# Performance work log

Measured on AMD Instinct MI355X. Metric: run time of the kernel, lower is better.

## Reference

```python
import jax, jax.numpy as jnp
import numpy as np

T, B, IN_DIM, H = 512, 256, 512, 256  # H == hidden_dim == n_qubits

def setup_inputs() -> dict:
    key = jax.random.key(0)
    ks = jax.random.split(key, 13)
    inputs = jax.random.normal(ks[0], (T, B, IN_DIM), dtype=jnp.float32)
    d = IN_DIM + H
    s = 1.0 / np.sqrt(d)
    def lin(k):
        k1, k2 = jax.random.split(k)
        return (jax.random.uniform(k1, (H, d), jnp.float32, -s, s),
                jax.random.uniform(k2, (H,), jnp.float32, -s, s))
    Wf, bf = lin(ks[1]); Wi, bi = lin(ks[2]); Wg, bg = lin(ks[3]); Wo, bo = lin(ks[4])
    thf = jax.random.uniform(ks[5], (H,), jnp.float32)
    thi = jax.random.uniform(ks[6], (H,), jnp.float32)
    thg = jax.random.uniform(ks[7], (H,), jnp.float32)
    tho = jax.random.uniform(ks[8], (H,), jnp.float32)
    return dict(inputs=inputs, Wf=Wf, bf=bf, thf=thf, Wi=Wi, bi=bi, thi=thi,
                Wg=Wg, bg=bg, thg=thg, Wo=Wo, bo=bo, tho=tho)

def _qgate(combined, W, b, th):
    # Analytic form of the RY+RY+CNOT-ladder circuit with PauliZ expvals:
    # <Z_k> = prod_{i<=k} cos(z_i + theta_i), z = Linear(combined)
    z = combined @ W.T + b  # [B, H]
    return jnp.cumprod(jnp.cos(z + th), axis=-1)

def reference(inputs, Wf, bf, thf, Wi, bi, thi, Wg, bg, thg, Wo, bo, tho):
    batch = inputs.shape[1]
    hx0 = jnp.zeros((batch, H), inputs.dtype)
    cx0 = jnp.zeros((batch, H), inputs.dtype)

    def step(carry, x):
        hx, cx = carry
        comb = jnp.concatenate([x, hx], axis=1)  # [B, IN_DIM+H]
        f = jax.nn.sigmoid(_qgate(comb, Wf, bf, thf))
        i = jax.nn.sigmoid(_qgate(comb, Wi, bi, thi))
        g = jnp.tanh(_qgate(comb, Wg, bg, thg))
        o = jax.nn.sigmoid(_qgate(comb, Wo, bo, tho))
        cx = f * cx + i * g
        hx = o * jnp.tanh(cx)
        return (hx, cx), hx

    (hx, cx), stacked = jax.lax.scan(step, (hx0, cx0), inputs)
    return stacked, hx, cx
```

## Files before the change

### kernel.cpp

```cpp
#include <hip/hip_runtime.h>
#include <hip/hip_bf16.h>
#include <stdint.h>

#define T_STEPS 512
#define BATCH   256
#define HID     256

#define NRWG   128
#define NWWG   128
#define NWG    256
#define RING   4
#define CHUNK  8
#define NCHUNK 64
#define TPC    64
#define SLOT_F (CHUNK*256*1024)

using short8 = __attribute__((ext_vector_type(8))) short;
using f32x4  = __attribute__((ext_vector_type(4))) float;

#define VMCNT0() asm volatile("s_waitcnt vmcnt(0)" ::: "memory")

__device__ inline unsigned short f2bf(float f) {
  unsigned u = __float_as_uint(f);
  unsigned r = (u + 0x7fffu + ((u >> 16) & 1u)) >> 16;
  return (unsigned short)r;
}
__device__ inline float sigm(float x)   { return __builtin_amdgcn_rcpf(1.0f + __expf(-x)); }
__device__ inline float tanh_f(float x) { return 2.0f * __builtin_amdgcn_rcpf(1.0f + __expf(-2.0f * x)) - 1.0f; }

__device__ inline int ld_rlx(const int* p) {
  return __hip_atomic_load(p, __ATOMIC_RELAXED, __HIP_MEMORY_SCOPE_AGENT);
}
__device__ inline void add_rlx(int* p, int v) {
  __hip_atomic_fetch_add(p, v, __ATOMIC_RELAXED, __HIP_MEMORY_SCOPE_AGENT);
}
__device__ inline float ldg_coh(const float* p) {
  return __hip_atomic_load(p, __ATOMIC_RELAXED, __HIP_MEMORY_SCOPE_AGENT);
}
__device__ inline void stg_coh(float* p, float v) {
  __hip_atomic_store(p, v, __ATOMIC_RELAXED, __HIP_MEMORY_SCOPE_AGENT);
}
__device__ inline void st16_coh(float* p, f32x4 v) {
  asm volatile("global_store_dwordx4 %0, %1, off sc0 sc1" :: "v"(p), "v"(v) : "memory");
}

__device__ inline int hswz(int byte) { return byte ^ (((byte >> 8) & 3) << 4); }

__global__ __launch_bounds__(256) void prep_kernel(
    const float* __restrict__ Wf, const float* __restrict__ Wi,
    const float* __restrict__ Wg, const float* __restrict__ Wo,
    const float* __restrict__ bf_, const float* __restrict__ bi_,
    const float* __restrict__ bg_, const float* __restrict__ bo_,
    const float* __restrict__ thf, const float* __restrict__ thi,
    const float* __restrict__ thg, const float* __restrict__ tho,
    unsigned short* __restrict__ Wfull, float* __restrict__ cvec,
    int* __restrict__ flags, float* __restrict__ pk)
{
  int j = blockIdx.x;
  int g = j >> 8, col = j & 255;
  const float* W  = (g==0)?Wf:(g==1)?Wi:(g==2)?Wg:Wo;
  const float* bb = (g==0)?bf_:(g==1)?bi_:(g==2)?bg_:bo_;
  const float* th = (g==0)?thf:(g==1)?thi:(g==2)?thg:tho;
  const float* wrow = W + (size_t)col * 768;
  for (int k = threadIdx.x; k < 768; k += blockDim.x)
    Wfull[(size_t)j * 768 + k] = f2bf(wrow[k]);
  if (threadIdx.x == 0) cvec[j] = bb[col] + th[col];
  if (j == 0) for (int i = threadIdx.x; i < 512; i += 256) flags[i] = 0;
  float* pz = pk + (size_t)j * 1024;
  for (int i = threadIdx.x; i < 1024; i += 256) pz[i] = 0.0f;
}

__global__ __launch_bounds__(512, 2) void persist_kernel(
    const float* __restrict__ X,
    const unsigned short* __restrict__ Wfull,
    const float* __restrict__ cvec,
    float* __restrict__ ring,
    float* __restrict__ pk,
    int* __restrict__ done,
    int* __restrict__ consumed,
    float* __restrict__ out)
{
  __shared__ union {
    struct { unsigned short hL[4096]; float z[8][1032]; int rdy[2]; } rec;
    struct { unsigned short aL[4096]; unsigned short bL[8192]; } gem;
  } sm;

  int bid = blockIdx.x, tid = threadIdx.x;
  int lane = tid & 63, wv = tid >> 6;
  int l15 = lane & 15, lk = lane >> 4;

  if (bid < NRWG) {
    int bg = bid >> 2, g = bid & 3;

    for (int i = tid; i < 4096; i += 512) sm.rec.hL[i] = 0;
    if (tid == 0) { sm.rec.rdy[0] = 0; sm.rec.rdy[1] = 0; }

    short8 af[2][8];
#pragma unroll
    for (int ti = 0; ti < 2; ++ti)
#pragma unroll
      for (int kk = 0; kk < 8; ++kk)
        af[ti][kk] = *(const short8*)(Wfull +
            (size_t)(g*256 + wv*32 + ti*16 + l15)*768 + 512 + kk*32 + lk*8);

    float creg[4] = {0.f, 0.f, 0.f, 0.f};
    float zx[4];
    bool pf_prev = false;
    __syncthreads();

    for (int t = 0; t < T_STEPS; ++t) {
      int cIdx = t >> 3;
      if ((t & 7) == 0 && !pf_prev) {
        if (tid == 0) { while (ld_rlx(&done[cIdx]) < TPC) __builtin_amdgcn_s_sleep(1); }
        __syncthreads();
        const float* zp = ring + (size_t)(cIdx & (RING-1))*SLOT_F
                        + ((size_t)(t & 7)*256 + bg*8 + wv)*1024 + g*256 + lane;
#pragma unroll
        for (int s = 0; s < 4; ++s) zx[s] = ldg_coh(zp + s*64);
      }

      short8 bfr[8];
#pragma unroll
      for (int kk = 0; kk < 8; ++kk)
        bfr[kk] = *(const short8*)((const char*)sm.rec.hL + hswz(kk*1024 + lane*16));
      f32x4 acc0 = {0.f,0.f,0.f,0.f}, acc1 = {0.f,0.f,0.f,0.f};
#pragma unroll
      for (int kk = 0; kk < 8; ++kk) {
        acc0 = __builtin_amdgcn_mfma_f32_16x16x32_bf16(af[0][kk], bfr[kk], acc0, 0, 0, 0);
        acc1 = __builtin_amdgcn_mfma_f32_16x16x32_bf16(af[1][kk], bfr[kk], acc1, 0, 0, 0);
      }
      if (l15 < 8) {
        *(f32x4*)&sm.rec.z[l15][wv*32 +      lk*4] = acc0;
        *(f32x4*)&sm.rec.z[l15][wv*32 + 16 + lk*4] = acc1;
      }
      __syncthreads();

      float v[4];
#pragma unroll
      for (int s = 0; s < 4; ++s)
        v[s] = __cosf(sm.rec.z[wv][s*64 + lane] + zx[s]);
#pragma unroll
      for (int off = 1; off < 64; off <<= 1) {
        float u0 = __shfl_up(v[0], (unsigned)off, 64);
        float u1 = __shfl_up(v[1], (unsigned)off, 64);
        float u2 = __shfl_up(v[2], (unsigned)off, 64);
        float u3 = __shfl_up(v[3], (unsigned)off, 64);
        if (lane >= off) { v[0]*=u0; v[1]*=u1; v[2]*=u2; v[3]*=u3; }
      }
      float t0 = __shfl(v[0], 63, 64), t1 = __shfl(v[1], 63, 64), t2 = __shfl(v[2], 63, 64);
      float p1 = t0, p2 = t0*t1, p3 = p2*t2;
      float a0 = v[0], a1 = v[1]*p1, a2 = v[2]*p2, a3 = v[3]*p3;
      float act[4];
      if (g == 2) { act[0]=tanh_f(a0); act[1]=tanh_f(a1); act[2]=tanh_f(a2); act[3]=tanh_f(a3); }
      else        { act[0]=sigm(a0);   act[1]=sigm(a1);   act[2]=sigm(a2);   act[3]=sigm(a3); }

      int par = t & 1, T1 = t + 1;
      float seqf = __int_as_float(T1);
      float* myb = pk + ((((size_t)par*32 + bg)*4 + g)*8 + wv)*512 + (size_t)lane*8;
      f32x4 P1 = {act[0], act[1], act[2], seqf};
      f32x4 P2 = {act[3], seqf, 0.f, 0.f};
      st16_coh(myb, P1);
      st16_coh(myb + 4, P2);

      int rdyv = sm.rec.rdy[par];
      bool pf = (((t+1) & 7) == 0) && (t+1 < T_STEPS) && (rdyv >= TPC);
      if (tid == 0) {
        int cn = cIdx + 1;
        sm.rec.rdy[par ^ 1] = ld_rlx(&done[cn]);
      }
      if (t+1 < T_STEPS && (((t+1) & 7) != 0 || pf)) {
        int cN = (t+1) >> 3;
        const float* zp = ring + (size_t)(cN & (RING-1))*SLOT_F
                        + ((size_t)((t+1) & 7)*256 + bg*8 + wv)*1024 + g*256 + lane;
#pragma unroll
        for (int s = 0; s < 4; ++s) zx[s] = ldg_coh(zp + s*64);
      }
      pf_prev = pf;

      int q0 = (g+1)&3, q1 = (g+2)&3, q2 = (g+3)&3;
      const float* A1 = pk + ((((size_t)par*32 + bg)*4 + q0)*8 + wv)*512 + (size_t)lane*8;
      const float* B1 = pk + ((((size_t)par*32 + bg)*4 + q1)*8 + wv)*512 + (size_t)lane*8;
      const float* C1 = pk + ((((size_t)par*32 + bg)*4 + q2)*8 + wv)*512 + (size_t)lane*8;
      f32x4 qa1, qa2, qb1, qb2, qc1, qc2;
      while (true) {
        asm volatile(
          "global_load_dwordx4 %0, %6,  off sc0 sc1\n\t"
          "global_load_dwordx4 %1, %7,  off sc0 sc1\n\t"
          "global_load_dwordx4 %2, %8,  off sc0 sc1\n\t"
          "global_load_dwordx4 %3, %9,  off sc0 sc1\n\t"
          "global_load_dwordx4 %4, %10, off sc0 sc1\n\t"
          "global_load_dwordx4 %5, %11, off sc0 sc1\n\t"
          "s_waitcnt vmcnt(0)"
          : "=&v"(qa1), "=&v"(qa2), "=&v"(qb1), "=&v"(qb2), "=&v"(qc1), "=&v"(qc2)
          : "v"(A1), "v"(A1+4), "v"(B1), "v"(B1+4), "v"(C1), "v"(C1+4)
          : "memory");
        if (__float_as_int(qa1[3]) >= T1 && __float_as_int(qa2[1]) >= T1 &&
            __float_as_int(qb1[3]) >= T1 && __float_as_int(qb2[1]) >= T1 &&
            __float_as_int(qc1[3]) >= T1 && __float_as_int(qc2[1]) >= T1) break;
      }

      float vals[4][4];
#pragma unroll
      for (int s = 0; s < 4; ++s) vals[g][s] = act[s];
      vals[q0][0]=qa1[0]; vals[q0][1]=qa1[1]; vals[q0][2]=qa1[2]; vals[q0][3]=qa2[0];
      vals[q1][0]=qb1[0]; vals[q1][1]=qb1[1]; vals[q1][2]=qb1[2]; vals[q1][3]=qb2[0];
      vals[q2][0]=qc1[0]; vals[q2][1]=qc1[1]; vals[q2][2]=qc1[2]; vals[q2][3]=qc2[0];

      int brow = bg*8 + wv;
#pragma unroll
      for (int s = 0; s < 4; ++s) {
        float cn = vals[0][s]*creg[s] + vals[1][s]*vals[2][s];
        creg[s] = cn;
        float h = vals[3][s]*tanh_f(cn);
        int k = s*64 + lane;
        int byte = (k >> 5)*1024 + ((((k >> 3) & 3)*16 + wv)*16) + (k & 7)*2;
        *(unsigned short*)((char*)sm.rec.hL + hswz(byte)) = f2bf(h);
        if (g == 0) {
          out[(size_t)t*(BATCH*HID) + (size_t)brow*256 + s*64 + lane] = h;
          if (t == T_STEPS-1) {
            out[(size_t)T_STEPS*(BATCH*HID) + (size_t)brow*256 + s*64 + lane] = h;
            out[(size_t)T_STEPS*(BATCH*HID) + BATCH*HID + (size_t)brow*256 + s*64 + lane] = cn;
          }
        }
      }
      if ((t & 7) == 7 && tid == 0) add_rlx(consumed, 1);
      __syncthreads();
    }
  } else {
    int w0 = bid - NRWG;
    int wr = wv >> 2, wc = wv & 3;
    int rA = tid >> 2, kA = (tid & 3) * 8;
    int rB = tid >> 1, kB = (tid & 1) * 16;

    for (int gt = w0; gt < NCHUNK * TPC; gt += NWWG) {
      int c  = gt >> 6;
      int tl = gt & 63;
      int tm = tl >> 2, tn = tl & 3;

      int need = NRWG * (c - RING + 1);
      if (need > 0) {
        if (tid == 0) { while (ld_rlx(consumed) < need) __builtin_amdgcn_s_sleep(8); }
        __syncthreads();
      }

      const float* Xb = X + ((size_t)c*(CHUNK*256) + (size_t)tm*128) * 512;
      float* slotp = ring + (size_t)(c & (RING-1)) * SLOT_F;

      f32x4 acc[4][4];
#pragma unroll
      for (int mi = 0; mi < 4; ++mi)
#pragma unroll
        for (int ni = 0; ni < 4; ++ni) acc[mi][ni] = (f32x4){0.f,0.f,0.f,0.f};

      int slotA = (rA >> 4)*1024 + ((tid & 3)*16 + (rA & 15))*16;
      int baseB = (rB >> 4)*1024;
      int kO = kB >> 3;
      int slotB0 = baseB + ((kO    )*16 + (rB & 15))*16;
      int slotB1 = baseB + ((kO + 1)*16 + (rB & 15))*16;

      for (int kb = 0; kb < 512; kb += 32) {
        const float* ap = Xb + (size_t)rA*512 + kb + kA;
        f32x4 v0 = *(const f32x4*)ap;
        f32x4 v1 = *(const f32x4*)(ap + 4);
        unsigned short t8[8];
        t8[0]=f2bf(v0[0]); t8[1]=f2bf(v0[1]); t8[2]=f2bf(v0[2]); t8[3]=f2bf(v0[3]);
        t8[4]=f2bf(v1[0]); t8[5]=f2bf(v1[1]); t8[6]=f2bf(v1[2]); t8[7]=f2bf(v1[3]);
        *(short8*)((char*)sm.gem.aL + slotA) = *(short8*)t8;
        const unsigned short* bp = Wfull + (size_t)(tn*256 + rB)*768 + kb + kB;
        *(short8*)((char*)sm.gem.bL + slotB0) = *(const short8*)bp;
        *(short8*)((char*)sm.gem.bL + slotB1) = *(const short8*)(bp + 8);
        __syncthreads();

        short8 afr[4], bfr4[4];
#pragma unroll
        for (int mi = 0; mi < 4; ++mi)
          afr[mi]  = *(const short8*)((const char*)sm.gem.aL + (wr*4 + mi)*1024 + lane*16);
#pragma unroll
        for (int ni = 0; ni < 4; ++ni)
          bfr4[ni] = *(const short8*)((const char*)sm.gem.bL + (wc*4 + ni)*1024 + lane*16);
#pragma unroll
        for (int mi = 0; mi < 4; ++mi)
#pragma unroll
          for (int ni = 0; ni < 4; ++ni)
            acc[mi][ni] = __builtin_amdgcn_mfma_f32_16x16x32_bf16(afr[mi], bfr4[ni], acc[mi][ni], 0, 0, 0);
        __syncthreads();
      }

#pragma unroll
      for (int mi = 0; mi < 4; ++mi) {
#pragma unroll
        for (int ni = 0; ni < 4; ++ni) {
          int col = tn*256 + wc*64 + ni*16 + l15;
          float cv = cvec[col];
#pragma unroll
          for (int reg = 0; reg < 4; ++reg) {
            int row = tm*128 + wr*64 + mi*16 + lk*4 + reg;
            stg_coh(&slotp[(size_t)row*1024 + col], acc[mi][ni][reg] + cv);
          }
        }
      }
      VMCNT0();
      __syncthreads();
      if (tid == 0) add_rlx(&done[c], 1);
    }
  }
}

extern "C" void kernel_launch(void* const* d_in, const int* in_sizes, int n_in,
                              void* d_out, int out_size, void* d_ws, size_t ws_size,
                              hipStream_t stream) {
  const float* x   = (const float*)d_in[0];
  const float* Wf  = (const float*)d_in[1];
  const float* bf_ = (const float*)d_in[2];
  const float* thf = (const float*)d_in[3];
  const float* Wi  = (const float*)d_in[4];
  const float* bi_ = (const float*)d_in[5];
  const float* thi = (const float*)d_in[6];
  const float* Wg  = (const float*)d_in[7];
  const float* bg_ = (const float*)d_in[8];
  const float* thg = (const float*)d_in[9];
  const float* Wo  = (const float*)d_in[10];
  const float* bo_ = (const float*)d_in[11];
  const float* tho = (const float*)d_in[12];
  float* out = (float*)d_out;

  char* ws = (char*)d_ws;
  unsigned short* Wfull = (unsigned short*)ws;
  float* cvec  = (float*)(ws + 1572864);
  int*   flags = (int*)(ws + 1576960);
  float* pk    = (float*)(ws + 2097152);
  float* ring  = (float*)(ws + 8388608);

  prep_kernel<<<1024, 256, 0, stream>>>(Wf, Wi, Wg, Wo, bf_, bi_, bg_, bo_,
                                        thf, thi, thg, tho, Wfull, cvec, flags, pk);
  persist_kernel<<<NWG, 512, 0, stream>>>(x, Wfull, cvec, ring, pk,
                                          flags, flags + 128, out);
}
```

Before: 2.623 ms.

## Halve recurrent workgroups per batch group, each computing two gates

Each recurrent workgroup now computes two gates (f,i or g,o) for its 8 batch rows instead of one. The cross-workgroup gate exchange drops from polling three peers to polling a single partner, and the exchange record is packed into three 16-byte stores. The freed workgroups are reassigned to the input-projection GEMM producers, and the early-prefetch logic at chunk boundaries is removed. In exchange, each recurrent workgroup does twice the MFMA, cos, scan and activation work per step on the serial critical path.

```diff
diff --git a/kernel.cpp b/kernel.cpp
--- a/kernel.cpp
+++ b/kernel.cpp
@@ -6,8 +6,8 @@
 #define BATCH   256
 #define HID     256
 
-#define NRWG   128
-#define NWWG   128
+#define NRWG   64
+#define NWWG   192
 #define NWG    256
 #define RING   4
 #define CHUNK  8
@@ -40,11 +40,17 @@
 __device__ inline void stg_coh(float* p, float v) {
   __hip_atomic_store(p, v, __ATOMIC_RELAXED, __HIP_MEMORY_SCOPE_AGENT);
 }
-__device__ inline void st16_coh(float* p, f32x4 v) {
+__device__ inline void st16_coh(f32x4* p, f32x4 v) {
   asm volatile("global_store_dwordx4 %0, %1, off sc0 sc1" :: "v"(p), "v"(v) : "memory");
 }
 
 __device__ inline int hswz(int byte) { return byte ^ (((byte >> 8) & 3) << 4); }
+
+struct RecSm {
+  unsigned short hL[4096];
+  float z[8][520];
+};
+struct GemSm { unsigned short aL[4096]; unsigned short bL[8192]; };
 
 __global__ __launch_bounds__(256) void prep_kernel(
     const float* __restrict__ Wf, const float* __restrict__ Wi,
@@ -66,8 +72,8 @@
     Wfull[(size_t)j * 768 + k] = f2bf(wrow[k]);
   if (threadIdx.x == 0) cvec[j] = bb[col] + th[col];
   if (j == 0) for (int i = threadIdx.x; i < 512; i += 256) flags[i] = 0;
-  float* pz = pk + (size_t)j * 1024;
-  for (int i = threadIdx.x; i < 1024; i += 256) pz[i] = 0.0f;
+  float* pz = pk + (size_t)j * 768;
+  for (int i = threadIdx.x; i < 768; i += 256) pz[i] = 0.0f;
 }
 
 __global__ __launch_bounds__(512, 2) void persist_kernel(
@@ -75,151 +81,154 @@
     const unsigned short* __restrict__ Wfull,
     const float* __restrict__ cvec,
     float* __restrict__ ring,
-    float* __restrict__ pk,
+    f32x4* __restrict__ pk,
     int* __restrict__ done,
     int* __restrict__ consumed,
     float* __restrict__ out)
 {
-  __shared__ union {
-    struct { unsigned short hL[4096]; float z[8][1032]; int rdy[2]; } rec;
-    struct { unsigned short aL[4096]; unsigned short bL[8192]; } gem;
-  } sm;
+  __shared__ union { RecSm rec; GemSm gem; } sm;
 
   int bid = blockIdx.x, tid = threadIdx.x;
   int lane = tid & 63, wv = tid >> 6;
   int l15 = lane & 15, lk = lane >> 4;
 
   if (bid < NRWG) {
-    int bg = bid >> 2, g = bid & 3;
+    int bg = bid >> 1, half = bid & 1;
 
     for (int i = tid; i < 4096; i += 512) sm.rec.hL[i] = 0;
-    if (tid == 0) { sm.rec.rdy[0] = 0; sm.rec.rdy[1] = 0; }
-
-    short8 af[2][8];
-#pragma unroll
-    for (int ti = 0; ti < 2; ++ti)
+
+    short8 af[4][8];
+#pragma unroll
+    for (int st = 0; st < 4; ++st)
 #pragma unroll
       for (int kk = 0; kk < 8; ++kk)
-        af[ti][kk] = *(const short8*)(Wfull +
-            (size_t)(g*256 + wv*32 + ti*16 + l15)*768 + 512 + kk*32 + lk*8);
+        af[st][kk] = *(const short8*)(Wfull +
+            (size_t)(half*512 + wv*64 + st*16 + l15)*768 + 512 + kk*32 + lk*8);
 
     float creg[4] = {0.f, 0.f, 0.f, 0.f};
-    float zx[4];
-    bool pf_prev = false;
+    float zx[8];
     __syncthreads();
 
     for (int t = 0; t < T_STEPS; ++t) {
       int cIdx = t >> 3;
-      if ((t & 7) == 0 && !pf_prev) {
+      if ((t & 7) == 0) {
         if (tid == 0) { while (ld_rlx(&done[cIdx]) < TPC) __builtin_amdgcn_s_sleep(1); }
         __syncthreads();
         const float* zp = ring + (size_t)(cIdx & (RING-1))*SLOT_F
-                        + ((size_t)(t & 7)*256 + bg*8 + wv)*1024 + g*256 + lane;
-#pragma unroll
-        for (int s = 0; s < 4; ++s) zx[s] = ldg_coh(zp + s*64);
+                        + ((size_t)(bg*8 + wv))*1024 + half*512 + lane;
+#pragma unroll
+        for (int s = 0; s < 8; ++s) zx[s] = ldg_coh(zp + s*64);
       }
 
       short8 bfr[8];
 #pragma unroll
       for (int kk = 0; kk < 8; ++kk)
         bfr[kk] = *(const short8*)((const char*)sm.rec.hL + hswz(kk*1024 + lane*16));
-      f32x4 acc0 = {0.f,0.f,0.f,0.f}, acc1 = {0.f,0.f,0.f,0.f};
-#pragma unroll
-      for (int kk = 0; kk < 8; ++kk) {
-        acc0 = __builtin_amdgcn_mfma_f32_16x16x32_bf16(af[0][kk], bfr[kk], acc0, 0, 0, 0);
-        acc1 = __builtin_amdgcn_mfma_f32_16x16x32_bf16(af[1][kk], bfr[kk], acc1, 0, 0, 0);
-      }
+      f32x4 acc[4];
+#pragma unroll
+      for (int st = 0; st < 4; ++st) acc[st] = (f32x4){0.f,0.f,0.f,0.f};
+#pragma unroll
+      for (int kk = 0; kk < 8; ++kk)
+#pragma unroll
+        for (int st = 0; st < 4; ++st)
+          acc[st] = __builtin_amdgcn_mfma_f32_16x16x32_bf16(af[st][kk], bfr[kk], acc[st], 0, 0, 0);
       if (l15 < 8) {
-        *(f32x4*)&sm.rec.z[l15][wv*32 +      lk*4] = acc0;
-        *(f32x4*)&sm.rec.z[l15][wv*32 + 16 + lk*4] = acc1;
+#pragma unroll
+        for (int st = 0; st < 4; ++st)
+          *(f32x4*)&sm.rec.z[l15][wv*64 + st*16 + lk*4] = acc[st];
       }
       __syncthreads();
 
-      float v[4];
-#pragma unroll
-      for (int s = 0; s < 4; ++s)
+      float v[8];
+#pragma unroll
+      for (int s = 0; s < 8; ++s)
         v[s] = __cosf(sm.rec.z[wv][s*64 + lane] + zx[s]);
 #pragma unroll
       for (int off = 1; off < 64; off <<= 1) {
-        float u0 = __shfl_up(v[0], (unsigned)off, 64);
-        float u1 = __shfl_up(v[1], (unsigned)off, 64);
-        float u2 = __shfl_up(v[2], (unsigned)off, 64);
-        float u3 = __shfl_up(v[3], (unsigned)off, 64);
-        if (lane >= off) { v[0]*=u0; v[1]*=u1; v[2]*=u2; v[3]*=u3; }
-      }
-      float t0 = __shfl(v[0], 63, 64), t1 = __shfl(v[1], 63, 64), t2 = __shfl(v[2], 63, 64);
-      float p1 = t0, p2 = t0*t1, p3 = p2*t2;
-      float a0 = v[0], a1 = v[1]*p1, a2 = v[2]*p2, a3 = v[3]*p3;
-      float act[4];
-      if (g == 2) { act[0]=tanh_f(a0); act[1]=tanh_f(a1); act[2]=tanh_f(a2); act[3]=tanh_f(a3); }
-      else        { act[0]=sigm(a0);   act[1]=sigm(a1);   act[2]=sigm(a2);   act[3]=sigm(a3); }
+        float u[8];
+#pragma unroll
+        for (int s = 0; s < 8; ++s) u[s] = __shfl_up(v[s], (unsigned)off, 64);
+        if (lane >= off) {
+#pragma unroll
+          for (int s = 0; s < 8; ++s) v[s] *= u[s];
+        }
+      }
+      float tA0 = __shfl(v[0], 63, 64), tA1 = __shfl(v[1], 63, 64), tA2 = __shfl(v[2], 63, 64);
+      float tB0 = __shfl(v[4], 63, 64), tB1 = __shfl(v[5], 63, 64), tB2 = __shfl(v[6], 63, 64);
+      float pA2 = tA0*tA1, pA3 = pA2*tA2;
+      float pB2 = tB0*tB1, pB3 = pB2*tB2;
+      float aA[4] = {v[0], v[1]*tA0, v[2]*pA2, v[3]*pA3};
+      float aB[4] = {v[4], v[5]*tB0, v[6]*pB2, v[7]*pB3};
+      if (half == 0) {
+#pragma unroll
+        for (int s = 0; s < 4; ++s) { aA[s] = sigm(aA[s]); aB[s] = sigm(aB[s]); }
+      } else {
+#pragma unroll
+        for (int s = 0; s < 4; ++s) { aA[s] = tanh_f(aA[s]); aB[s] = sigm(aB[s]); }
+      }
 
       int par = t & 1, T1 = t + 1;
       float seqf = __int_as_float(T1);
-      float* myb = pk + ((((size_t)par*32 + bg)*4 + g)*8 + wv)*512 + (size_t)lane*8;
-      f32x4 P1 = {act[0], act[1], act[2], seqf};
-      f32x4 P2 = {act[3], seqf, 0.f, 0.f};
-      st16_coh(myb, P1);
-      st16_coh(myb + 4, P2);
-
-      int rdyv = sm.rec.rdy[par];
-      bool pf = (((t+1) & 7) == 0) && (t+1 < T_STEPS) && (rdyv >= TPC);
-      if (tid == 0) {
-        int cn = cIdx + 1;
-        sm.rec.rdy[par ^ 1] = ld_rlx(&done[cn]);
-      }
-      if (t+1 < T_STEPS && (((t+1) & 7) != 0 || pf)) {
-        int cN = (t+1) >> 3;
-        const float* zp = ring + (size_t)(cN & (RING-1))*SLOT_F
-                        + ((size_t)((t+1) & 7)*256 + bg*8 + wv)*1024 + g*256 + lane;
-#pragma unroll
-        for (int s = 0; s < 4; ++s) zx[s] = ldg_coh(zp + s*64);
-      }
-      pf_prev = pf;
-
-      int q0 = (g+1)&3, q1 = (g+2)&3, q2 = (g+3)&3;
-      const float* A1 = pk + ((((size_t)par*32 + bg)*4 + q0)*8 + wv)*512 + (size_t)lane*8;
-      const float* B1 = pk + ((((size_t)par*32 + bg)*4 + q1)*8 + wv)*512 + (size_t)lane*8;
-      const float* C1 = pk + ((((size_t)par*32 + bg)*4 + q2)*8 + wv)*512 + (size_t)lane*8;
-      f32x4 qa1, qa2, qb1, qb2, qc1, qc2;
-      while (true) {
+      size_t idx = ((((size_t)par*32 + bg)*2 + half)*8 + wv)*64 + lane;
+      f32x4* myp = pk + idx*3;
+      f32x4 P0 = {aA[0], aA[1], aA[2], seqf};
+      f32x4 P1 = {aA[3], aB[0], aB[1], seqf};
+      f32x4 P2 = {aB[2], aB[3], 0.f,  seqf};
+      st16_coh(myp,     P0);
+      st16_coh(myp + 1, P1);
+      st16_coh(myp + 2, P2);
+
+      if (((t+1) & 7) != 0 && t+1 < T_STEPS) {
+        const float* zp = ring + (size_t)(cIdx & (RING-1))*SLOT_F
+                        + ((size_t)(((t+1) & 7)*256) + bg*8 + wv)*1024 + half*512 + lane;
+#pragma unroll
+        for (int s = 0; s < 8; ++s) zx[s] = ldg_coh(zp + s*64);
+      }
+
+      size_t pidx = ((((size_t)par*32 + bg)*2 + (half^1))*8 + wv)*64 + lane;
+      const f32x4* pp = pk + pidx*3;
+      f32x4 q0, q1, q2;
+      do {
         asm volatile(
-          "global_load_dwordx4 %0, %6,  off sc0 sc1\n\t"
-          "global_load_dwordx4 %1, %7,  off sc0 sc1\n\t"
-          "global_load_dwordx4 %2, %8,  off sc0 sc1\n\t"
-          "global_load_dwordx4 %3, %9,  off sc0 sc1\n\t"
-          "global_load_dwordx4 %4, %10, off sc0 sc1\n\t"
-          "global_load_dwordx4 %5, %11, off sc0 sc1\n\t"
+          "global_load_dwordx4 %0, %3, off sc0 sc1\n\t"
+          "global_load_dwordx4 %1, %4, off sc0 sc1\n\t"
+          "global_load_dwordx4 %2, %5, off sc0 sc1\n\t"
           "s_waitcnt vmcnt(0)"
-          : "=&v"(qa1), "=&v"(qa2), "=&v"(qb1), "=&v"(qb2), "=&v"(qc1), "=&v"(qc2)
-          : "v"(A1), "v"(A1+4), "v"(B1), "v"(B1+4), "v"(C1), "v"(C1+4)
+          : "=&v"(q0), "=&v"(q1), "=&v"(q2)
+          : "v"(pp), "v"(pp + 1), "v"(pp + 2)
           : "memory");
-        if (__float_as_int(qa1[3]) >= T1 && __float_as_int(qa2[1]) >= T1 &&
-            __float_as_int(qb1[3]) >= T1 && __float_as_int(qb2[1]) >= T1 &&
-            __float_as_int(qc1[3]) >= T1 && __float_as_int(qc2[1]) >= T1) break;
-      }
-
-      float vals[4][4];
-#pragma unroll
-      for (int s = 0; s < 4; ++s) vals[g][s] = act[s];
-      vals[q0][0]=qa1[0]; vals[q0][1]=qa1[1]; vals[q0][2]=qa1[2]; vals[q0][3]=qa2[0];
-      vals[q1][0]=qb1[0]; vals[q1][1]=qb1[1]; vals[q1][2]=qb1[2]; vals[q1][3]=qb2[0];
-      vals[q2][0]=qc1[0]; vals[q2][1]=qc1[1]; vals[q2][2]=qc1[2]; vals[q2][3]=qc2[0];
+      } while (__float_as_int(q0[3]) < T1 || __float_as_int(q1[3]) < T1 ||
+               __float_as_int(q2[3]) < T1);
+      float p0 = q0[0], p1 = q0[1], p2 = q0[2], p3 = q1[0];
+      float p4 = q1[1], p5 = q1[2], p6 = q2[0], p7 = q2[1];
+
+      float fv[4], iv[4], gv[4], ov[4];
+      if (half == 0) {
+#pragma unroll
+        for (int s = 0; s < 4; ++s) { fv[s] = aA[s]; iv[s] = aB[s]; }
+        gv[0]=p0; gv[1]=p1; gv[2]=p2; gv[3]=p3;
+        ov[0]=p4; ov[1]=p5; ov[2]=p6; ov[3]=p7;
+      } else {
+#pragma unroll
+        for (int s = 0; s < 4; ++s) { gv[s] = aA[s]; ov[s] = aB[s]; }
+        fv[0]=p0; fv[1]=p1; fv[2]=p2; fv[3]=p3;
+        iv[0]=p4; iv[1]=p5; iv[2]=p6; iv[3]=p7;
+      }
 
       int brow = bg*8 + wv;
 #pragma unroll
       for (int s = 0; s < 4; ++s) {
-        float cn = vals[0][s]*creg[s] + vals[1][s]*vals[2][s];
+        float cn = fv[s]*creg[s] + iv[s]*gv[s];
         creg[s] = cn;
-        float h = vals[3][s]*tanh_f(cn);
+        float h = ov[s]*tanh_f(cn);
         int k = s*64 + lane;
         int byte = (k >> 5)*1024 + ((((k >> 3) & 3)*16 + wv)*16) + (k & 7)*2;
         *(unsigned short*)((char*)sm.rec.hL + hswz(byte)) = f2bf(h);
-        if (g == 0) {
-          out[(size_t)t*(BATCH*HID) + (size_t)brow*256 + s*64 + lane] = h;
+        if (half == 0) {
+          out[(size_t)t*(BATCH*HID) + (size_t)brow*256 + k] = h;
           if (t == T_STEPS-1) {
-            out[(size_t)T_STEPS*(BATCH*HID) + (size_t)brow*256 + s*64 + lane] = h;
-            out[(size_t)T_STEPS*(BATCH*HID) + BATCH*HID + (size_t)brow*256 + s*64 + lane] = cn;
+            out[(size_t)T_STEPS*(BATCH*HID) + (size_t)brow*256 + k] = h;
+            out[(size_t)T_STEPS*(BATCH*HID) + BATCH*HID + (size_t)brow*256 + k] = cn;
           }
         }
       }
@@ -328,11 +337,12 @@
   unsigned short* Wfull = (unsigned short*)ws;
   float* cvec  = (float*)(ws + 1572864);
   int*   flags = (int*)(ws + 1576960);
-  float* pk    = (float*)(ws + 2097152);
+  f32x4* pk    = (f32x4*)(ws + 2097152);
   float* ring  = (float*)(ws + 8388608);
 
   prep_kernel<<<1024, 256, 0, stream>>>(Wf, Wi, Wg, Wo, bf_, bi_, bg_, bo_,
-                                        thf, thi, thg, tho, Wfull, cvec, flags, pk);
+                                        thf, thi, thg, tho, Wfull, cvec, flags,
+                                        (float*)pk);
   persist_kernel<<<NWG, 512, 0, stream>>>(x, Wfull, cvec, ring, pk,
                                           flags, flags + 128, out);
 }
```

After: 2.712 ms. 3.4% more time.
